# Kernel optimization log

Hardware: AMD Instinct MI355X
Metric: run time of the kernel (lower is better)

## Reference

```python
import jax, jax.numpy as jnp
from jax import lax
import numpy as np

NPOINT = 1024
RADIUS = 0.25
NSAMPLE = 32
USE_XYZ = True


def setup_inputs() -> dict:
    key = jax.random.key(0)
    k1, k2 = jax.random.split(key)
    xyz = jax.random.normal(k1, (8, 8192, 3), dtype=jnp.float32)
    points = jax.random.normal(k2, (8, 8192, 32), dtype=jnp.float32)
    return {"xyz": xyz, "points": points}


def furthest_point_sample(xyz, npoint):
    """Iterative FPS; returns (B, npoint, 3) sampled coordinates.
    Matches torch reference: seeded with xyz[:, 0], squared-distance metric."""
    B, N, _ = xyz.shape
    first = xyz[:, 0]  # (B, 3)
    d0 = jnp.full((B, N), 1e38, dtype=xyz.dtype)

    def step(carry, _):
        dist, last = carry  # dist: (B,N), last: (B,3)
        d2 = jnp.sum((xyz - last[:, None, :]) ** 2, axis=-1)  # (B,N)
        dist = jnp.minimum(dist, d2)
        idx = jnp.argmax(dist, axis=1)  # (B,)
        nxt = jnp.take_along_axis(xyz, idx[:, None, None], axis=1)[:, 0]  # (B,3)
        return (dist, nxt), nxt

    _, outs = lax.scan(step, (d0, first), None, length=npoint - 1)  # (npoint-1, B, 3)
    return jnp.concatenate([first[None], outs], axis=0).transpose(1, 0, 2)  # (B,npoint,3)


def ball_query(radius, nsample, xyz, new_xyz):
    """First `nsample` indices within `radius` of each center (ascending index
    order), padded with the first found index — matches pointnet2 CUDA kernel.
    Returns (B, npoint, nsample) int32."""
    N = xyz.shape[1]
    d2 = jnp.sum((new_xyz[:, :, None, :] - xyz[:, None, :, :]) ** 2, axis=-1)  # (B,npoint,N)
    mask = d2 < radius * radius
    ar = jnp.arange(N, dtype=jnp.int32)
    # top_k on negated indices -> smallest valid indices first
    score = jnp.where(mask, -ar, jnp.int32(-(N + 1)))
    vals, _ = lax.top_k(score, nsample)  # (B,npoint,nsample), descending
    valid = vals > -(N + 1)
    idx = jnp.where(valid, -vals, -vals[..., :1])  # pad with first hit
    return idx.astype(jnp.int32)


def group_points(points, idx):
    """points (B,N,C), idx (B,npoint,nsample) -> (B,npoint,nsample,C)."""
    B, npoint, nsample = idx.shape
    C = points.shape[-1]
    flat = idx.reshape(B, npoint * nsample)  # (B, npoint*nsample)
    g = jnp.take_along_axis(points, flat[:, :, None], axis=1)
    return g.reshape(B, npoint, nsample, C)


def reference(xyz, points):
    new_xyz = furthest_point_sample(xyz, NPOINT)  # (B,npoint,3)
    idx = ball_query(RADIUS, NSAMPLE, xyz, new_xyz)  # (B,npoint,nsample)
    grouped_xyz = group_points(xyz, idx) - new_xyz[:, :, None, :]  # center-relative
    grouped_points = group_points(points, idx)
    if USE_XYZ:
        new_points = jnp.concatenate([grouped_xyz, grouped_points], axis=-1)
    else:
        new_points = grouped_points
    return new_xyz, new_points
```

## Files before the change

### kernel.cpp

```cpp
#include <hip/hip_runtime.h>

#define BATCH   8
#define NPTS    8192
#define NPOINT  1024
#define NSAMPLE 32
#define CHANC   32
#define OUTC    35
#define R2      0.0625f

typedef float v2f __attribute__((ext_vector_type(2)));

template <int CTRL>
__device__ __forceinline__ float dpp_max_step(float v) {
    int r = __builtin_amdgcn_update_dpp(__float_as_int(v), __float_as_int(v),
                                        CTRL, 0xf, 0xf, false);
    return fmaxf(v, __int_as_float(r));
}
#define DPP_ROW_SHR(n)  (0x110 | (n))
#define DPP_BCAST15     0x142
#define DPP_BCAST31     0x143

__global__ __launch_bounds__(512) void fps_kernel(const float* __restrict__ xyz,
                                                  float* __restrict__ new_xyz) {
#pragma clang fp contract(off)
    const int b    = blockIdx.x;
    const int t    = threadIdx.x;
    const int lane = t & 63;
    const int w    = t >> 6;
    const float* bx = xyz + (size_t)b * NPTS * 3;

    __shared__ float4 pts[NPTS];
    __shared__ __align__(16) float pv[2][8];
    __shared__ __align__(16) int   pi[2][8];

    v2f px[8], py[8], pz[8], dist[8];
    {
        float f[48];
        float4* fq = (float4*)f;
        const float4* s4 = (const float4*)bx + t * 12;
#pragma unroll
        for (int q = 0; q < 12; ++q) fq[q] = s4[q];
#pragma unroll
        for (int p = 0; p < 8; ++p) {
            px[p] = (v2f){f[6 * p + 0], f[6 * p + 3]};
            py[p] = (v2f){f[6 * p + 1], f[6 * p + 4]};
            pz[p] = (v2f){f[6 * p + 2], f[6 * p + 5]};
            dist[p] = (v2f){1e38f, 1e38f};
        }
#pragma unroll
        for (int i = 0; i < 16; ++i) {
            const int j  = t * 16 + i;
            const int js = j ^ ((j >> 4) & 7);
            pts[js] = make_float4(f[3 * i + 0], f[3 * i + 1], f[3 * i + 2], 0.0f);
        }
    }
    __syncthreads();

    float4 c0 = pts[0];
    float lx = c0.x, ly = c0.y, lz = c0.z;
    if (t == 0) {
        float* o = new_xyz + (size_t)b * NPOINT * 3;
        o[0] = lx; o[1] = ly; o[2] = lz;
    }

    for (int s = 1; s < NPOINT; ++s) {
        const v2f lx2 = (v2f){lx, lx};
        const v2f ly2 = (v2f){ly, ly};
        const v2f lz2 = (v2f){lz, lz};
        float bestv = -1.0f;
        int   bi    = 0;
#pragma unroll
        for (int p = 0; p < 8; ++p) {
            const v2f dx = px[p] - lx2;
            const v2f dy = py[p] - ly2;
            const v2f dz = pz[p] - lz2;
            const v2f d2 = (dx * dx + dy * dy) + dz * dz;
            const float d0 = fminf(dist[p].x, d2.x);
            const float d1 = fminf(dist[p].y, d2.y);
            dist[p] = (v2f){d0, d1};
            if (d0 > bestv) { bestv = d0; bi = 2 * p; }
            if (d1 > bestv) { bestv = d1; bi = 2 * p + 1; }
        }
        const int besti = (t << 4) + bi;

        float v = bestv;
        v = dpp_max_step<DPP_ROW_SHR(1)>(v);
        v = dpp_max_step<DPP_ROW_SHR(2)>(v);
        v = dpp_max_step<DPP_ROW_SHR(4)>(v);
        v = dpp_max_step<DPP_ROW_SHR(8)>(v);
        v = dpp_max_step<DPP_BCAST15>(v);
        v = dpp_max_step<DPP_BCAST31>(v);
        const float smax = __int_as_float(__builtin_amdgcn_readlane(__float_as_int(v), 63));

        const unsigned long long m = __ballot(bestv == smax);
        const int par = s & 1;
        if (lane == (int)__builtin_ctzll(m)) {
            pv[par][w] = smax;
            pi[par][w] = besti;
        }
        __syncthreads();

        const float4* pvq = (const float4*)pv[par];
        const float4 a = pvq[0];
        const float4 c = pvq[1];
        const float M = fmaxf(fmaxf(fmaxf(a.x, a.y), fmaxf(a.z, a.w)),
                              fmaxf(fmaxf(c.x, c.y), fmaxf(c.z, c.w)));
        const unsigned mask = (unsigned)(a.x == M)        | ((unsigned)(a.y == M) << 1)
                            | ((unsigned)(a.z == M) << 2) | ((unsigned)(a.w == M) << 3)
                            | ((unsigned)(c.x == M) << 4) | ((unsigned)(c.y == M) << 5)
                            | ((unsigned)(c.z == M) << 6) | ((unsigned)(c.w == M) << 7);
        const int slot = __builtin_ctz(mask);
        const int idx  = pi[par][slot];

        const int js = idx ^ ((idx >> 4) & 7);
        const float4 cw = pts[js];
        lx = cw.x; ly = cw.y; lz = cw.z;
        if (t == 0) {
            float* o = new_xyz + ((size_t)b * NPOINT + s) * 3;
            o[0] = lx; o[1] = ly; o[2] = lz;
        }
    }
}

__global__ __launch_bounds__(256) void ballgroup_kernel(const float* __restrict__ xyz,
                                                        const float* __restrict__ points,
                                                        const float* __restrict__ new_xyz,
                                                        float* __restrict__ out) {
#pragma clang fp contract(off)
    const int lane = threadIdx.x & 63;
    const int w    = threadIdx.x >> 6;
    const int gw   = blockIdx.x * 4 + w;
    const int b    = gw >> 10;

    const float* bx  = xyz + (size_t)b * NPTS * 3;
    const float* cen = new_xyz + (size_t)gw * 3;
    const float cx = cen[0], cy = cen[1], cz = cen[2];

    __shared__ int idxbuf[4][NSAMPLE];

    int k = 0;
    for (int base = 0; base < NPTS; base += 128) {
        const int j0 = base + lane;
        const int j1 = j0 + 64;
        const float a0 = bx[j0 * 3 + 0], a1 = bx[j0 * 3 + 1], a2 = bx[j0 * 3 + 2];
        const float c0 = bx[j1 * 3 + 0], c1 = bx[j1 * 3 + 1], c2 = bx[j1 * 3 + 2];
        const float dxa = a0 - cx, dya = a1 - cy, dza = a2 - cz;
        const float d2a = (dxa * dxa + dya * dya) + dza * dza;
        const float dxb = c0 - cx, dyb = c1 - cy, dzb = c2 - cz;
        const float d2b = (dxb * dxb + dyb * dyb) + dzb * dzb;
        const bool inA = d2a < R2;
        const bool inB = d2b < R2;

        const unsigned long long mA = __ballot(inA);
        int pre = __popcll(mA & ((1ull << lane) - 1ull));
        if (inA && (k + pre) < NSAMPLE) idxbuf[w][k + pre] = j0;
        k += __popcll(mA);
        if (k >= NSAMPLE) { k = NSAMPLE; break; }

        const unsigned long long mB = __ballot(inB);
        pre = __popcll(mB & ((1ull << lane) - 1ull));
        if (inB && (k + pre) < NSAMPLE) idxbuf[w][k + pre] = j1;
        k += __popcll(mB);
        if (k >= NSAMPLE) { k = NSAMPLE; break; }
    }
    const int first = idxbuf[w][0];

    float*       o    = out + (size_t)gw * NSAMPLE * OUTC;
    const float* prow = points + (size_t)b * NPTS * CHANC;
    for (int e = lane; e < NSAMPLE * OUTC; e += 64) {
        const int s = e / OUTC;
        const int c = e - s * OUTC;
        const int j = (s < k) ? idxbuf[w][s] : first;
        float v;
        if (c < 3) {
            const float cc = (c == 0) ? cx : (c == 1) ? cy : cz;
            v = bx[j * 3 + c] - cc;
        } else {
            v = prow[j * CHANC + (c - 3)];
        }
        o[e] = v;
    }
}

extern "C" void kernel_launch(void* const* d_in, const int* in_sizes, int n_in,
                              void* d_out, int out_size, void* d_ws, size_t ws_size,
                              hipStream_t stream) {
    const float* xyz    = (const float*)d_in[0];
    const float* points = (const float*)d_in[1];
    float* new_xyz    = (float*)d_out;
    float* new_points = new_xyz + (size_t)BATCH * NPOINT * 3;

    fps_kernel<<<BATCH, 512, 0, stream>>>(xyz, new_xyz);
    ballgroup_kernel<<<(BATCH * NPOINT) / 4, 256, 0, stream>>>(xyz, points, new_xyz, new_points);
}
```

Baseline: 1.122 ms.

## Carry winner coordinates in FPS reduction instead of indexing shared point table

Removes the 128KB shared-memory copy of all points from the FPS kernel. Each thread now picks its local winner's coordinates from registers with a select tree, and each wave publishes (x,y,z,dist) as a float4, so the next centre comes straight out of the 8-entry partial array. This drops one dependent LDS lookup per iteration from the serial critical path, and the per-thread max is rebuilt as a balanced tree plus an equality mask. The cost is extra select instructions per step, and lower register pressure is not guaranteed.

```diff
diff --git a/kernel.cpp b/kernel.cpp
--- a/kernel.cpp
+++ b/kernel.cpp
@@ -20,8 +20,8 @@
 #define DPP_BCAST15     0x142
 #define DPP_BCAST31     0x143
 
-__global__ __launch_bounds__(512) void fps_kernel(const float* __restrict__ xyz,
-                                                  float* __restrict__ new_xyz) {
+__global__ __launch_bounds__(512, 1) void fps_kernel(const float* __restrict__ xyz,
+                                                     float* __restrict__ new_xyz) {
 #pragma clang fp contract(off)
     const int b    = blockIdx.x;
     const int t    = threadIdx.x;
@@ -29,9 +29,7 @@
     const int w    = t >> 6;
     const float* bx = xyz + (size_t)b * NPTS * 3;
 
-    __shared__ float4 pts[NPTS];
-    __shared__ __align__(16) float pv[2][8];
-    __shared__ __align__(16) int   pi[2][8];
+    __shared__ __align__(16) float4 part[2][8];
 
     v2f px[8], py[8], pz[8], dist[8];
     {
@@ -47,17 +45,9 @@
             pz[p] = (v2f){f[6 * p + 2], f[6 * p + 5]};
             dist[p] = (v2f){1e38f, 1e38f};
         }
-#pragma unroll
-        for (int i = 0; i < 16; ++i) {
-            const int j  = t * 16 + i;
-            const int js = j ^ ((j >> 4) & 7);
-            pts[js] = make_float4(f[3 * i + 0], f[3 * i + 1], f[3 * i + 2], 0.0f);
-        }
-    }
-    __syncthreads();
-
-    float4 c0 = pts[0];
-    float lx = c0.x, ly = c0.y, lz = c0.z;
+    }
+
+    float lx = bx[0], ly = bx[1], lz = bx[2];
     if (t == 0) {
         float* o = new_xyz + (size_t)b * NPOINT * 3;
         o[0] = lx; o[1] = ly; o[2] = lz;
@@ -67,8 +57,7 @@
         const v2f lx2 = (v2f){lx, lx};
         const v2f ly2 = (v2f){ly, ly};
         const v2f lz2 = (v2f){lz, lz};
-        float bestv = -1.0f;
-        int   bi    = 0;
+        float d[16];
 #pragma unroll
         for (int p = 0; p < 8; ++p) {
             const v2f dx = px[p] - lx2;
@@ -78,10 +67,37 @@
             const float d0 = fminf(dist[p].x, d2.x);
             const float d1 = fminf(dist[p].y, d2.y);
             dist[p] = (v2f){d0, d1};
-            if (d0 > bestv) { bestv = d0; bi = 2 * p; }
-            if (d1 > bestv) { bestv = d1; bi = 2 * p + 1; }
-        }
-        const int besti = (t << 4) + bi;
+            d[2 * p] = d0; d[2 * p + 1] = d1;
+        }
+
+        float m8[8], m4[4], m2[2];
+#pragma unroll
+        for (int q = 0; q < 8; ++q) m8[q] = fmaxf(d[2 * q], d[2 * q + 1]);
+#pragma unroll
+        for (int q = 0; q < 4; ++q) m4[q] = fmaxf(m8[2 * q], m8[2 * q + 1]);
+        m2[0] = fmaxf(m4[0], m4[1]); m2[1] = fmaxf(m4[2], m4[3]);
+        const float bestv = fmaxf(m2[0], m2[1]);
+        unsigned lm = 0;
+#pragma unroll
+        for (int i = 0; i < 16; ++i) lm |= ((unsigned)(d[i] == bestv)) << i;
+        const int bi = (int)__builtin_ctz(lm);
+
+        const int g = bi >> 1;
+        v2f ax0 = (g & 1) ? px[1] : px[0], ax1 = (g & 1) ? px[3] : px[2];
+        v2f ax2 = (g & 1) ? px[5] : px[4], ax3 = (g & 1) ? px[7] : px[6];
+        v2f ay0 = (g & 1) ? py[1] : py[0], ay1 = (g & 1) ? py[3] : py[2];
+        v2f ay2 = (g & 1) ? py[5] : py[4], ay3 = (g & 1) ? py[7] : py[6];
+        v2f az0 = (g & 1) ? pz[1] : pz[0], az1 = (g & 1) ? pz[3] : pz[2];
+        v2f az2 = (g & 1) ? pz[5] : pz[4], az3 = (g & 1) ? pz[7] : pz[6];
+        v2f bx0 = (g & 2) ? ax1 : ax0, bx1 = (g & 2) ? ax3 : ax2;
+        v2f by0 = (g & 2) ? ay1 : ay0, by1 = (g & 2) ? ay3 : ay2;
+        v2f bz0 = (g & 2) ? az1 : az0, bz1 = (g & 2) ? az3 : az2;
+        const v2f cxv = (g & 4) ? bx1 : bx0;
+        const v2f cyv = (g & 4) ? by1 : by0;
+        const v2f czv = (g & 4) ? bz1 : bz0;
+        const float wx = (bi & 1) ? cxv.y : cxv.x;
+        const float wy = (bi & 1) ? cyv.y : cyv.x;
+        const float wz = (bi & 1) ? czv.y : czv.x;
 
         float v = bestv;
         v = dpp_max_step<DPP_ROW_SHR(1)>(v);
@@ -95,25 +111,27 @@
         const unsigned long long m = __ballot(bestv == smax);
         const int par = s & 1;
         if (lane == (int)__builtin_ctzll(m)) {
-            pv[par][w] = smax;
-            pi[par][w] = besti;
+            part[par][w] = make_float4(wx, wy, wz, smax);
         }
         __syncthreads();
 
-        const float4* pvq = (const float4*)pv[par];
-        const float4 a = pvq[0];
-        const float4 c = pvq[1];
-        const float M = fmaxf(fmaxf(fmaxf(a.x, a.y), fmaxf(a.z, a.w)),
-                              fmaxf(fmaxf(c.x, c.y), fmaxf(c.z, c.w)));
-        const unsigned mask = (unsigned)(a.x == M)        | ((unsigned)(a.y == M) << 1)
-                            | ((unsigned)(a.z == M) << 2) | ((unsigned)(a.w == M) << 3)
-                            | ((unsigned)(c.x == M) << 4) | ((unsigned)(c.y == M) << 5)
-                            | ((unsigned)(c.z == M) << 6) | ((unsigned)(c.w == M) << 7);
-        const int slot = __builtin_ctz(mask);
-        const int idx  = pi[par][slot];
-
-        const int js = idx ^ ((idx >> 4) & 7);
-        const float4 cw = pts[js];
+        const float4* P = part[par];
+        const float4 q0 = P[0], q1 = P[1], q2 = P[2], q3 = P[3];
+        const float4 q4 = P[4], q5 = P[5], q6 = P[6], q7 = P[7];
+        const float M = fmaxf(fmaxf(fmaxf(q0.w, q1.w), fmaxf(q2.w, q3.w)),
+                              fmaxf(fmaxf(q4.w, q5.w), fmaxf(q6.w, q7.w)));
+        const unsigned mk = (unsigned)(q0.w == M)        | ((unsigned)(q1.w == M) << 1)
+                          | ((unsigned)(q2.w == M) << 2) | ((unsigned)(q3.w == M) << 3)
+                          | ((unsigned)(q4.w == M) << 4) | ((unsigned)(q5.w == M) << 5)
+                          | ((unsigned)(q6.w == M) << 6) | ((unsigned)(q7.w == M) << 7);
+        const int slot = (int)__builtin_ctz(mk);
+        const float4 a0 = (slot & 1) ? q1 : q0;
+        const float4 a1 = (slot & 1) ? q3 : q2;
+        const float4 a2 = (slot & 1) ? q5 : q4;
+        const float4 a3 = (slot & 1) ? q7 : q6;
+        const float4 b0 = (slot & 2) ? a1 : a0;
+        const float4 b1 = (slot & 2) ? a3 : a2;
+        const float4 cw = (slot & 4) ? b1 : b0;
         lx = cw.x; ly = cw.y; lz = cw.z;
         if (t == 0) {
             float* o = new_xyz + ((size_t)b * NPOINT + s) * 3;
```

Result: slower. 1.754 ms (+56.3%).
